# Kernel optimization log

Measured on AMD Instinct MI355X. Metric: run time of the kernel, lower is better.

## Reference

```python
import jax, jax.numpy as jnp
import numpy as np

B, T, D, A, H, NA = 32, 256, 1024, 64, 512, 20


def setup_inputs() -> dict:
    key = jax.random.key(0)
    ks = jax.random.split(key, 20)
    g = lambda i, sh: jax.random.normal(ks[i], sh, dtype=jnp.float32) * 0.05
    z = lambda sh: jnp.zeros(sh, jnp.float32)
    return dict(
        sentence=jax.random.normal(ks[0], (B, T, D), dtype=jnp.float32),
        actions=jax.random.randint(ks[1], (B, T), 0, NA),
        token_empty=g(2, (D,)),
        leaf_Wi=g(3, (D, D)), leaf_bi=z((D,)),
        leaf_Wo=g(4, (D, D)), leaf_bo=z((D,)),
        lstm_Wih=g(5, (4 * D, D)), lstm_Whh=g(6, (4 * D, D)),
        lstm_bih=z((4 * D,)), lstm_bhh=z((4 * D,)),
        stack_h0=g(7, (D,)), stack_c0=g(8, (D,)),
        act_emb=g(9, (NA, A)),
        act_Wih=g(10, (4 * D, A)), act_Whh=g(11, (4 * D, D)),
        act_bih=z((4 * D,)), act_bhh=z((4 * D,)),
        act_h0=g(12, (D,)), act_c0=g(13, (D,)),
        red_W=g(14, (4, D, 2 * D)), red_b=z((4, D)),
        h2f_W=g(15, (H, 8 * D)), h2f_b=z((H,)),
        f2a_W=g(16, (NA, H)), f2a_b=z((NA,)),
        att_W=g(17, (3, D, D)),
    )


def _lstm_cell(x, h, c, Wih, Whh, bih, bhh):
    # torch.nn.LSTMCell math
    gates = x @ Wih.T + bih + h @ Whh.T + bhh
    i, f, g, o = jnp.split(gates, 4, axis=-1)
    c2 = jax.nn.sigmoid(f) * c + jax.nn.sigmoid(i) * jnp.tanh(g)
    return jax.nn.sigmoid(o) * jnp.tanh(c2), c2


def _forward(sentence, token_empty, leaf_Wi, leaf_bi, leaf_Wo, leaf_bo,
             lstm_Wih, lstm_Whh, lstm_bih, lstm_bhh, stack_h0, stack_c0,
             act_emb, act_Wih, act_Whh, act_bih, act_bhh, act_h0, act_c0,
             red_W, red_b, h2f_W, h2f_b, f2a_W, f2a_b, att_W, actions):
    # _LeafModule on every token, vectorized: [B,T,D]
    cell = jnp.einsum('btd,ed->bte', sentence, leaf_Wi) + leaf_bi
    hid = jax.nn.sigmoid(jnp.einsum('btd,ed->bte', sentence, leaf_Wo) + leaf_bo) * jnp.tanh(cell)
    hid_t = jnp.swapaxes(hid, 0, 1)    # [T,B,D]
    cell_t = jnp.swapaxes(cell, 0, 1)

    # stack-LSTM: push every leaf hidden (SHIFT sequence)
    def stack_step(carry, x_t):
        h, c = carry
        h2, c2 = _lstm_cell(x_t, h, c, lstm_Wih, lstm_Whh, lstm_bih, lstm_bhh)
        return (h2, c2), h2
    init = (jnp.broadcast_to(stack_h0, (B, D)), jnp.broadcast_to(stack_c0, (B, D)))
    (hf, cf), stack_hs = jax.lax.scan(stack_step, init, hid_t)

    # _ReduceModule tree-LSTM, left-to-right binary reduce over all leaves
    def red_step(carry, rt):
        lh, lc = carry
        rh, rc = rt
        cat = jnp.concatenate([lh, rh], axis=-1)  # [B,2D]
        ig = jax.nn.sigmoid(cat @ red_W[0].T + red_b[0])
        lg = jax.nn.sigmoid(cat @ red_W[1].T + red_b[1])
        rg = jax.nn.sigmoid(cat @ red_W[2].T + red_b[2])
        cand = jnp.tanh(cat @ red_W[3].T + red_b[3])
        c2 = ig * cand + lg * lc + rg * rc
        return (jnp.tanh(c2), c2), None
    (red_h, _), _ = jax.lax.scan(red_step, (hid_t[0], cell_t[0]), (hid_t[1:], cell_t[1:]))

    # push the reduced node onto the stack-LSTM; top3 of the stack
    s1, _ = _lstm_cell(red_h, hf, cf, lstm_Wih, lstm_Whh, lstm_bih, lstm_bhh)
    s2, s3 = stack_hs[-1], stack_hs[-2]

    # action-LSTM over the action history
    a_in = jnp.swapaxes(act_emb[actions], 0, 1)  # [T,B,A]
    def act_step(carry, x_t):
        h, c = carry
        h2, c2 = _lstm_cell(x_t, h, c, act_Wih, act_Whh, act_bih, act_bhh)
        return (h2, c2), None
    ainit = (jnp.broadcast_to(act_h0, (B, D)), jnp.broadcast_to(act_c0, (B, D)))
    (a_top, _), _ = jax.lax.scan(act_step, ainit, a_in)

    # bilinear attention of each stack summary over the encoded sentence
    def bilin(s, W):
        w = jax.nn.softmax(jnp.einsum('bd,de,bte->bt', s, W, sentence), axis=-1)
        return jnp.einsum('bt,btd->bd', w, sentence)
    att1, att2, att3 = bilin(s1, att_W[0]), bilin(s2, att_W[1]), bilin(s3, att_W[2])

    buf_top = jnp.broadcast_to(token_empty, (B, D))  # buffer exhausted -> empty state
    feat = jnp.concatenate([s1, s2, s3, buf_top, a_top, att1, att2, att3], axis=-1)  # [B,8D]
    logits = jnp.tanh(feat @ h2f_W.T + h2f_b) @ f2a_W.T + f2a_b
    return jax.nn.log_softmax(logits, axis=-1)  # [B,NA]


def reference(sentence, actions, token_empty, leaf_Wi, leaf_bi, leaf_Wo, leaf_bo,
              lstm_Wih, lstm_Whh, lstm_bih, lstm_bhh, stack_h0, stack_c0,
              act_emb, act_Wih, act_Whh, act_bih, act_bhh, act_h0, act_c0,
              red_W, red_b, h2f_W, h2f_b, f2a_W, f2a_b, att_W):
    return _forward(sentence, token_empty, leaf_Wi, leaf_bi, leaf_Wo, leaf_bo,
                    lstm_Wih, lstm_Whh, lstm_bih, lstm_bhh, stack_h0, stack_c0,
                    act_emb, act_Wih, act_Whh, act_bih, act_bhh, act_h0, act_c0,
                    red_W, red_b, h2f_W, h2f_b, f2a_W, f2a_b, att_W, actions)
```

## Files before the change

### kernel.cpp

```cpp
#include <hip/hip_runtime.h>
#include <hip/hip_bf16.h>
#include <math.h>

#define DEV __device__ __forceinline__

typedef __bf16 bf16_t;
typedef bf16_t bf16x8 __attribute__((ext_vector_type(8)));
typedef float f32x4 __attribute__((ext_vector_type(4)));
typedef int i32x4 __attribute__((ext_vector_type(4)));

DEV void async16(const void* g, void* l) {
  __builtin_amdgcn_global_load_lds((const __attribute__((address_space(1))) void*)g,
                                   (__attribute__((address_space(3))) void*)l, 16, 0, 0);
}
DEV float sigmoidf_(float x) { return 1.f / (1.f + expf(-x)); }
DEV bf16x8 as_bf(i32x4 v) { union { i32x4 i; bf16x8 b; } u; u.i = v; return u.b; }

DEV unsigned flag_load(const unsigned* p) {
  unsigned v;
  asm volatile("global_load_dword %0, %1, off sc0 sc1\ns_waitcnt vmcnt(0)"
               : "=v"(v) : "v"(p) : "memory");
  return v;
}
DEV void flag_store(unsigned* p, unsigned v) {
  asm volatile("global_store_dword %0, %1, off sc0 sc1" :: "v"(p), "v"(v) : "memory");
}
DEV void store16_sys(void* p, i32x4 v) {
  asm volatile("global_store_dwordx4 %0, %1, off sc0 sc1" :: "v"(p), "v"(v) : "memory");
}

#define WAITV(N) do { asm volatile("s_waitcnt vmcnt(" #N ")" ::: "memory"); \
                      __builtin_amdgcn_sched_barrier(0); } while (0)

template<int KB>
DEV void loads8(i32x4* dst, const __hip_bfloat16* arow) {
#pragma unroll
  for (int i = 0; i < 8; ++i)
    asm volatile("global_load_dwordx4 %0, %1, off offset:%2"
                 : "=v"(dst[i]) : "v"(arow), "i"((KB + i) * 64));
}
DEV void loads8rt(i32x4* dst, const __hip_bfloat16* arow, int kbase) {
#pragma unroll
  for (int i = 0; i < 8; ++i)
    asm volatile("global_load_dwordx4 %0, %1, off"
                 : "=v"(dst[i]) : "v"(arow + (size_t)(kbase + i) * 32) : "memory");
}

template<int C>
DEV void ldsb8(bf16x8* b0, bf16x8* b1, const __hip_bfloat16* Wl,
               int sw, int kof, int r0, int r1) {
#pragma unroll
  for (int i = 0; i < 8; ++i) {
    const int kk = (C * 8 + i) * 32 + kof;
    b0[i] = *(const bf16x8*)&Wl[r0 * 1024 + (kk ^ sw)];
    b1[i] = *(const bf16x8*)&Wl[r1 * 1024 + (kk ^ sw)];
  }
}
DEV void mfma8x(const i32x4* a, const bf16x8* b0, const bf16x8* b1,
                f32x4& acc0, f32x4& acc1) {
#pragma unroll
  for (int i = 0; i < 8; ++i) {
    bf16x8 av = as_bf(a[i]);
    acc0 = __builtin_amdgcn_mfma_f32_16x16x32_bf16(av, b0[i], acc0, 0, 0, 0);
    acc1 = __builtin_amdgcn_mfma_f32_16x16x32_bf16(av, b1[i], acc1, 0, 0, 0);
  }
}

DEV void mfma_step(const __hip_bfloat16* Ap, const __hip_bfloat16* Wl,
                   int mh, int nh, int l, f32x4& acc0, f32x4& acc1) {
  const __hip_bfloat16* arow = Ap + (mh * 16 + (l & 15)) * 1024 + (l >> 4) * 8;
  const int sw = (l & 7) << 3, kof = (l >> 4) * 8;
  const int r0 = nh * 32 + (l & 15), r1 = r0 + 16;
  i32x4 A0[8], A1[8], A2[8], A3[8];
  bf16x8 Ba0[8], Ba1[8], Bb0[8], Bb1[8];
  loads8<0>(A0, arow);
  loads8<8>(A1, arow);
  loads8<16>(A2, arow);
  loads8<24>(A3, arow);
  ldsb8<0>(Ba0, Ba1, Wl, sw, kof, r0, r1);
  WAITV(24);
  mfma8x(A0, Ba0, Ba1, acc0, acc1);
  ldsb8<1>(Bb0, Bb1, Wl, sw, kof, r0, r1);
  WAITV(16);
  mfma8x(A1, Bb0, Bb1, acc0, acc1);
  ldsb8<2>(Ba0, Ba1, Wl, sw, kof, r0, r1);
  WAITV(8);
  mfma8x(A2, Ba0, Ba1, acc0, acc1);
  ldsb8<3>(Bb0, Bb1, Wl, sw, kof, r0, r1);
  WAITV(0);
  mfma8x(A3, Bb0, Bb1, acc0, acc1);
}

DEV void mfma_pass_glb(const __hip_bfloat16* Ap, const __hip_bfloat16* __restrict__ Wg,
                       int d0, int mh, int nh, int l, f32x4& acc0, f32x4& acc1) {
  const __hip_bfloat16* arow = Ap + (mh * 16 + (l & 15)) * 1024 + (l >> 4) * 8;
  const size_t g0 = ((size_t)(2 * nh) * 1024 + d0 + (l & 15)) * 1024;
  const size_t g1 = g0 + 1048576;
  const int kof = (l >> 4) * 8;
  i32x4 A[8];
  for (int c = 0; c < 4; ++c) {
    loads8rt(A, arow, c * 8);
    WAITV(0);
#pragma unroll
    for (int i = 0; i < 8; ++i) {
      const int kk = (c * 8 + i) * 32 + kof;
      bf16x8 b0 = *(const bf16x8*)&Wg[g0 + kk];
      bf16x8 b1 = *(const bf16x8*)&Wg[g1 + kk];
      bf16x8 av = as_bf(A[i]);
      acc0 = __builtin_amdgcn_mfma_f32_16x16x32_bf16(av, b0, acc0, 0, 0, 0);
      acc1 = __builtin_amdgcn_mfma_f32_16x16x32_bf16(av, b1, acc1, 0, 0, 0);
    }
  }
}

__global__ __launch_bounds__(256) void gemm_bt_kernel(
    const __hip_bfloat16* __restrict__ A, const __hip_bfloat16* __restrict__ Bw,
    float* __restrict__ outF, __hip_bfloat16* __restrict__ outBF,
    const float* __restrict__ bias, const float* __restrict__ aux,
    int M, int N, int K, int remap, int mode)
{
  __shared__ __hip_bfloat16 As[128 * 64];
  __shared__ __hip_bfloat16 Bs[128 * 64];
  __shared__ __hip_bfloat16 Cs[128 * 128];
  const int tid = threadIdx.x;
  const int w = tid >> 6, l = tid & 63;
  const int m0 = blockIdx.x * 128, n0 = blockIdx.y * 128;
  const int wm = (w >> 1) * 64, wn = (w & 1) * 64;
  const int row_s = tid >> 3, kc = tid & 7;
  f32x4 acc[4][4] = {};
  for (int k0 = 0; k0 < K; k0 += 64) {
    const __hip_bfloat16* ga = A + (size_t)(m0 + row_s) * K + k0 + kc * 8;
    const __hip_bfloat16* gb = Bw + (size_t)(n0 + row_s) * K + k0 + kc * 8;
    __hip_bfloat16* la = As + w * 512;
    __hip_bfloat16* lb = Bs + w * 512;
#pragma unroll
    for (int p = 0; p < 4; ++p) {
      async16(ga + (size_t)p * 32 * K, la + p * 2048);
      async16(gb + (size_t)p * 32 * K, lb + p * 2048);
    }
    __syncthreads();
#pragma unroll
    for (int kb = 0; kb < 2; ++kb) {
      bf16x8 af[4], bfr[4];
#pragma unroll
      for (int i = 0; i < 4; ++i)
        af[i] = *(const bf16x8*)&As[(wm + i * 16 + (l & 15)) * 64 + kb * 32 + (l >> 4) * 8];
#pragma unroll
      for (int j = 0; j < 4; ++j)
        bfr[j] = *(const bf16x8*)&Bs[(wn + j * 16 + (l & 15)) * 64 + kb * 32 + (l >> 4) * 8];
#pragma unroll
      for (int i = 0; i < 4; ++i)
#pragma unroll
        for (int j = 0; j < 4; ++j)
          acc[i][j] = __builtin_amdgcn_mfma_f32_16x16x32_bf16(af[i], bfr[j], acc[i][j], 0, 0, 0);
    }
    __syncthreads();
  }
  if (mode == 3) {
#pragma unroll
    for (int i = 0; i < 4; ++i)
#pragma unroll
      for (int j = 0; j < 4; ++j) {
        const int ncol = n0 + wn + j * 16 + (l & 15);
        const float bv = bias[ncol];
#pragma unroll
        for (int r = 0; r < 4; ++r) {
          const int lr = wm + i * 16 + (l >> 4) * 4 + r;
          Cs[lr * 128 + wn + j * 16 + (l & 15)] = __float2bfloat16(acc[i][j][r] + bv);
        }
      }
    __syncthreads();
    const int t0 = m0 >> 5, g = n0 >> 10, slot0 = (n0 & 1023) >> 4;
    const int grp = tid >> 6, li = tid & 63;
    const int b = li >> 1, half = li & 1;
#pragma unroll
    for (int sl = 0; sl < 8; ++sl) {
      bf16x8 vv = *(const bf16x8*)&Cs[(grp * 32 + b) * 128 + sl * 16 + half * 8];
      *(bf16x8*)&outBF[(((size_t)(slot0 + sl)) * 256 + t0 + grp) * 2048 +
                       g * 512 + b * 16 + half * 8] = vv;
    }
    return;
  }
#pragma unroll
  for (int i = 0; i < 4; ++i) {
#pragma unroll
    for (int j = 0; j < 4; ++j) {
      const int ncol = n0 + wn + j * 16 + (l & 15);
      const float bv = bias ? bias[ncol] : 0.f;
#pragma unroll
      for (int r = 0; r < 4; ++r) {
        int m = m0 + wm + i * 16 + (l >> 4) * 4 + r;
        int row = remap ? (((m & 255) << 5) | (m >> 8)) : m;
        float v = acc[i][j][r] + bv;
        if (mode == 0) {
          outF[(size_t)row * N + ncol] = v;
        } else if (mode == 1) {
          outBF[(size_t)row * N + ncol] = __float2bfloat16(v);
        } else {
          float cv = aux[(size_t)row * N + ncol];
          outBF[(size_t)row * N + ncol] = __float2bfloat16(sigmoidf_(v) * tanhf(cv));
        }
      }
    }
  }
}

__global__ __launch_bounds__(256) void cellblk_kernel(const float* __restrict__ cell,
                                                      __hip_bfloat16* __restrict__ blk)
{
  __shared__ __hip_bfloat16 ls[32 * 1024];
  const int t = blockIdx.x, tid = threadIdx.x;
  for (int i = tid; i < 32 * 1024; i += 256)
    ls[i] = __float2bfloat16(cell[(size_t)t * 32768 + i]);
  __syncthreads();
  const int e = tid * 2;
  const int b = e >> 4, dd = e & 15;
  for (int sl = 0; sl < 64; ++sl) {
    union { __hip_bfloat16 h[2]; unsigned u; } pk;
    pk.h[0] = ls[b * 1024 + sl * 16 + dd];
    pk.h[1] = ls[b * 1024 + sl * 16 + dd + 1];
    *(unsigned*)&blk[((size_t)sl * 256 + t) * 512 + e] = pk.u;
  }
}

struct PP {
  const __hip_bfloat16 *Whh_s, *Wih_s, *Whh_r, *Whh_a;
  const __hip_bfloat16 *xgs_blk, *xgr_blk;
  const __hip_bfloat16* cellblk;
  const float* table;
  const int* actions;
  const float *stack_c0, *act_c0, *sbias;
  __hip_bfloat16 *sh_hist, *rh_hist, *ah_hist;
  float *s1, *s2, *s3, *atop;
  unsigned int* flags;
};

__global__ __launch_bounds__(256, 1) void scan_persist(PP P)
{
  __shared__ __hip_bfloat16 Wl[64 * 1024];
  __shared__ float gsm[32][16][4];
  __shared__ __align__(16) __hip_bfloat16 hstage[32][16];
  const int bid = blockIdx.x;
  const int scan = bid >> 6;
  const int slot = bid & 63;
  const int d0 = slot * 16;
  const int tid = threadIdx.x;
  const int l = tid & 63, w = tid >> 6;
  const int mh = w >> 1, nh = w & 1;

  const __hip_bfloat16* Wg = (scan == 0) ? P.Whh_s : ((scan == 1) ? P.Whh_r : P.Whh_a);
  for (int idx = tid; idx < 64 * 128; idx += 256) {
    int r = idx >> 7, k = (idx & 127) * 8;
    int grow = ((r >> 4) << 10) + d0 + (r & 15);
    bf16x8 v = *(const bf16x8*)&Wg[(size_t)grow * 1024 + k];
    *(bf16x8*)&Wl[r * 1024 + (k ^ ((r & 7) << 3))] = v;
  }
  const int e0 = tid, e1 = tid + 256;
  const int b0_ = e0 >> 4, dd0 = e0 & 15, b1_ = e1 >> 4, dd1 = e1 & 15;
  float creg0, creg1;
  if (scan == 0)      { creg0 = P.stack_c0[d0 + dd0]; creg1 = P.stack_c0[d0 + dd1]; }
  else if (scan == 1) {
    creg0 = __bfloat162float(P.cellblk[(size_t)slot * 256 * 512 + b0_ * 16 + dd0]);
    creg1 = __bfloat162float(P.cellblk[(size_t)slot * 256 * 512 + b1_ * 16 + dd1]);
  }
  else                { creg0 = P.act_c0[d0 + dd0]; creg1 = P.act_c0[d0 + dd1]; }
  __syncthreads();

  __hip_bfloat16* hist = (scan == 0) ? P.sh_hist : ((scan == 1) ? P.rh_hist : P.ah_hist);
  unsigned int* Fb = P.flags + scan * 1024;
  const int Ns = (scan == 1) ? 255 : 256;
  const int mbase = mh * 16 + (l >> 4) * 4;

  for (int s = 0; s < Ns; ++s) {
    const __hip_bfloat16* Ap = hist + (size_t)s * 32768;
    __hip_bfloat16* Hout = hist + (size_t)(s + 1) * 32768;

    __hip_bfloat16 pg0, pg1, pg2, pg3, pg4, pg5, pg6, pg7;
    __hip_bfloat16 pcb0, pcb1;
    int pa0 = 0, pa1 = 0;
    pg0 = pg1 = pg2 = pg3 = pg4 = pg5 = pg6 = pg7 = __float2bfloat16(0.f);
    pcb0 = pcb1 = __float2bfloat16(0.f);
    if (scan == 0) {
      const __hip_bfloat16* x0 = P.xgs_blk + ((size_t)slot * 256 + s) * 2048 + b0_ * 16 + dd0;
      const __hip_bfloat16* x1 = P.xgs_blk + ((size_t)slot * 256 + s) * 2048 + b1_ * 16 + dd1;
      pg0 = x0[0]; pg1 = x0[512]; pg2 = x0[1024]; pg3 = x0[1536];
      pg4 = x1[0]; pg5 = x1[512]; pg6 = x1[1024]; pg7 = x1[1536];
    } else if (scan == 1) {
      const __hip_bfloat16* x0 = P.xgr_blk + ((size_t)slot * 256 + s + 1) * 2048 + b0_ * 16 + dd0;
      const __hip_bfloat16* x1 = P.xgr_blk + ((size_t)slot * 256 + s + 1) * 2048 + b1_ * 16 + dd1;
      pg0 = x0[0]; pg1 = x0[512]; pg2 = x0[1024]; pg3 = x0[1536];
      pg4 = x1[0]; pg5 = x1[512]; pg6 = x1[1024]; pg7 = x1[1536];
      pcb0 = P.cellblk[((size_t)slot * 256 + s + 1) * 512 + b0_ * 16 + dd0];
      pcb1 = P.cellblk[((size_t)slot * 256 + s + 1) * 512 + b1_ * 16 + dd1];
    } else {
      pa0 = P.actions[b0_ * 256 + s];
      pa1 = P.actions[b1_ * 256 + s];
    }
    __builtin_amdgcn_sched_barrier(0);

    f32x4 acc0 = {}, acc1 = {};
    mfma_step(Ap, Wl, mh, nh, l, acc0, acc1);
#pragma unroll
    for (int r = 0; r < 4; ++r) {
      gsm[mbase + r][l & 15][nh * 2 + 0] = acc0[r];
      gsm[mbase + r][l & 15][nh * 2 + 1] = acc1[r];
    }
    __syncthreads();
#pragma unroll
    for (int q = 0; q < 2; ++q) {
      const int b = q ? b1_ : b0_, dd = q ? dd1 : dd0;
      const int d = d0 + dd;
      float& creg = q ? creg1 : creg0;
      float g0 = gsm[b][dd][0], g1 = gsm[b][dd][1], g2 = gsm[b][dd][2], g3 = gsm[b][dd][3];
      if (scan == 1) {
        float ig = sigmoidf_(g0 + __bfloat162float(q ? pg4 : pg0));
        float lg = sigmoidf_(g1 + __bfloat162float(q ? pg5 : pg1));
        float rg = sigmoidf_(g2 + __bfloat162float(q ? pg6 : pg2));
        float cand = tanhf(g3 + __bfloat162float(q ? pg7 : pg3));
        float rcv = __bfloat162float(q ? pcb1 : pcb0);
        float c2 = ig * cand + lg * creg + rg * rcv;
        creg = c2;
        hstage[b][dd] = __float2bfloat16(tanhf(c2));
      } else {
        float bi0, bi1, bi2, bi3;
        if (scan == 0) {
          bi0 = __bfloat162float(q ? pg4 : pg0); bi1 = __bfloat162float(q ? pg5 : pg1);
          bi2 = __bfloat162float(q ? pg6 : pg2); bi3 = __bfloat162float(q ? pg7 : pg3);
        } else {
          int a = q ? pa1 : pa0;
          const float* tb = P.table + a * 4096;
          bi0 = tb[d]; bi1 = tb[1024 + d]; bi2 = tb[2048 + d]; bi3 = tb[3072 + d];
        }
        float c2 = sigmoidf_(g1 + bi1) * creg + sigmoidf_(g0 + bi0) * tanhf(g2 + bi2);
        float h2 = sigmoidf_(g3 + bi3) * tanhf(c2);
        creg = c2;
        hstage[b][dd] = __float2bfloat16(h2);
        if (scan == 0 && s == 254) P.s3[b * 1024 + d] = h2;
        if (scan == 0 && s == 255) P.s2[b * 1024 + d] = h2;
        if (scan == 2 && s == 255) P.atop[b * 1024 + d] = h2;
      }
    }
    __syncthreads();
    if (tid < 64) {
      const int bb = tid >> 1, hf = tid & 1;
      union { bf16x8 b8; i32x4 i4; } u;
      u.b8 = *(const bf16x8*)&hstage[bb][hf * 8];
      store16_sys(Hout + bb * 1024 + d0 + hf * 8, u.i4);
    }
    asm volatile("s_waitcnt vmcnt(0)" ::: "memory");
    __syncthreads();
    if (tid == 0) flag_store(Fb + slot * 16, (unsigned)(s + 1));
    if (tid < 64) {
      const unsigned tgt = (unsigned)(s + 1);
      if (flag_load(Fb + tid * 16) < tgt) {
        while (flag_load(Fb + tid * 16) < tgt) __builtin_amdgcn_s_sleep(1);
      }
    }
    __syncthreads();
  }

  if (scan == 0) {
    if (tid < 64) {
      while (flag_load(P.flags + 1024 + tid * 16) < 255u) __builtin_amdgcn_s_sleep(1);
    }
    __syncthreads();
    f32x4 acc0 = {}, acc1 = {};
    mfma_step(P.sh_hist + (size_t)256 * 32768, Wl, mh, nh, l, acc0, acc1);
    mfma_pass_glb(P.rh_hist + (size_t)255 * 32768, P.Wih_s, d0, mh, nh, l, acc0, acc1);
#pragma unroll
    for (int r = 0; r < 4; ++r) {
      gsm[mbase + r][l & 15][nh * 2 + 0] = acc0[r];
      gsm[mbase + r][l & 15][nh * 2 + 1] = acc1[r];
    }
    __syncthreads();
#pragma unroll
    for (int q = 0; q < 2; ++q) {
      const int b = q ? b1_ : b0_, dd = q ? dd1 : dd0;
      const int d = d0 + dd;
      float creg = q ? creg1 : creg0;
      float g0 = gsm[b][dd][0], g1 = gsm[b][dd][1], g2 = gsm[b][dd][2], g3 = gsm[b][dd][3];
      float bi0 = P.sbias[d], bi1 = P.sbias[1024 + d], bi2 = P.sbias[2048 + d], bi3 = P.sbias[3072 + d];
      float c2 = sigmoidf_(g1 + bi1) * creg + sigmoidf_(g0 + bi0) * tanhf(g2 + bi2);
      float h2 = sigmoidf_(g3 + bi3) * tanhf(c2);
      P.s1[b * 1024 + d] = h2;
    }
  }
}

__global__ void cast_kernel(__hip_bfloat16* dst, const float* src, int n) {
  int i = blockIdx.x * 256 + threadIdx.x;
  if (i < n) dst[i] = __float2bfloat16(src[i]);
}
__global__ void extract_half_kernel(__hip_bfloat16* dst, const float* src, int n,
                                    int src_stride, int src_off) {
  int i = blockIdx.x * 256 + threadIdx.x;
  if (i < n) {
    int r = i >> 10, k = i & 1023;
    dst[i] = __float2bfloat16(src[(size_t)r * src_stride + src_off + k]);
  }
}
__global__ void bias_kernel(float* dst, const float* a, const float* b, int n) {
  int i = blockIdx.x * 256 + threadIdx.x;
  if (i < n) dst[i] = a[i] + b[i];
}
__global__ void act_table_kernel(const float* emb, const float* Wih, const float* bih,
                                 const float* bhh, float* table) {
  int i = blockIdx.x * 256 + threadIdx.x;
  int a = i >> 12, n = i & 4095;
  float acc = bih[n] + bhh[n];
  const float* er = emb + a * 64;
  const float* wr = Wih + (size_t)n * 64;
  for (int k = 0; k < 64; ++k) acc += er[k] * wr[k];
  table[i] = acc;
}
__global__ void init_states_kernel(const float* stack_h0, const float* act_h0,
                                   const __hip_bfloat16* hid,
                                   __hip_bfloat16* sh0, __hip_bfloat16* ah0,
                                   __hip_bfloat16* rh0, unsigned int* flags)
{
  int i = blockIdx.x * 256 + threadIdx.x;
  int d = i & 1023;
  sh0[i] = __float2bfloat16(stack_h0[d]);
  ah0[i] = __float2bfloat16(act_h0[d]);
  rh0[i] = hid[i];
  if (i < 4096) flags[i] = 0u;
}

__global__ __launch_bounds__(256) void att_q_kernel(
    const float* s1, const float* s2, const float* s3, const float* attW, float* q)
{
  int eb = blockIdx.x, bg = blockIdx.y, j = blockIdx.z;
  const float* sj = (j == 0) ? s1 : ((j == 1) ? s2 : s3);
  __shared__ float ls[4][1024];
  int tid = threadIdx.x;
  for (int i = tid; i < 4096; i += 256)
    ls[i >> 10][i & 1023] = sj[(size_t)(bg * 4 + (i >> 10)) * 1024 + (i & 1023)];
  __syncthreads();
  int e = eb * 256 + tid;
  const float* Wj = attW + (size_t)j * 1024 * 1024;
  float a0 = 0, a1 = 0, a2 = 0, a3 = 0;
  for (int d = 0; d < 1024; ++d) {
    float wv = Wj[(size_t)d * 1024 + e];
    a0 += ls[0][d] * wv; a1 += ls[1][d] * wv; a2 += ls[2][d] * wv; a3 += ls[3][d] * wv;
  }
  q[((size_t)j * 32 + bg * 4 + 0) * 1024 + e] = a0;
  q[((size_t)j * 32 + bg * 4 + 1) * 1024 + e] = a1;
  q[((size_t)j * 32 + bg * 4 + 2) * 1024 + e] = a2;
  q[((size_t)j * 32 + bg * 4 + 3) * 1024 + e] = a3;
}

__global__ __launch_bounds__(256) void att_sc_kernel(const float* q, const float* sent, float* att)
{
  int b = blockIdx.x, j = blockIdx.y;
  __shared__ float qs[1024];
  __shared__ float wsm[256];
  __shared__ float red[8];
  int tid = threadIdx.x, w = tid >> 6, l = tid & 63;
  for (int i = tid; i < 1024; i += 256) qs[i] = q[((size_t)j * 32 + b) * 1024 + i];
  __syncthreads();
  const float* sp = sent + ((size_t)b * 256 + tid) * 1024;
  float dot = 0;
  for (int k = 0; k < 1024; ++k) dot += qs[k] * sp[k];
  float v = dot;
  for (int off = 32; off; off >>= 1) v = fmaxf(v, __shfl_xor(v, off));
  if (l == 0) red[w] = v;
  __syncthreads();
  float m = fmaxf(fmaxf(red[0], red[1]), fmaxf(red[2], red[3]));
  float ex = expf(dot - m);
  float sv = ex;
  for (int off = 32; off; off >>= 1) sv += __shfl_xor(sv, off);
  if (l == 0) red[4 + w] = sv;
  __syncthreads();
  float ssum = red[4] + red[5] + red[6] + red[7];
  wsm[tid] = ex / ssum;
  __syncthreads();
  for (int it = 0; it < 4; ++it) {
    int e = it * 256 + tid;
    float a = 0;
    for (int t2 = 0; t2 < 256; ++t2) a += wsm[t2] * sent[((size_t)b * 256 + t2) * 1024 + e];
    att[((size_t)j * 32 + b) * 1024 + e] = a;
  }
}

__global__ void feat_kernel(const float* s1, const float* s2, const float* s3,
                            const float* tok, const float* atop, const float* att, float* feat)
{
  int i = blockIdx.x * 256 + threadIdx.x;
  int b = i >> 13, jj = (i >> 10) & 7, d = i & 1023;
  int sidx = b * 1024 + d;
  float v;
  switch (jj) {
    case 0: v = s1[sidx]; break;
    case 1: v = s2[sidx]; break;
    case 2: v = s3[sidx]; break;
    case 3: v = tok[d]; break;
    case 4: v = atop[sidx]; break;
    default: v = att[((size_t)(jj - 5) * 32 + b) * 1024 + d];
  }
  feat[i] = v;
}
__global__ __launch_bounds__(256) void head_kernel(const float* feat, const float* W,
                                                   const float* bias, float* fbuf)
{
  int i = blockIdx.x * 256 + threadIdx.x;
  int b = i >> 9, h = i & 511;
  const float* fr = feat + (size_t)b * 8192;
  const float* wr = W + (size_t)h * 8192;
  float a = bias[h];
  for (int k = 0; k < 8192; ++k) a += fr[k] * wr[k];
  fbuf[i] = tanhf(a);
}
__global__ void logits_kernel(const float* fbuf, const float* W, const float* bias, float* out)
{
  int b = blockIdx.x, tid = threadIdx.x;
  __shared__ float lg[20];
  __shared__ float mred, lsred;
  if (tid < 20) {
    const float* fr = fbuf + b * 512;
    const float* wr = W + tid * 512;
    float a = bias[tid];
    for (int k = 0; k < 512; ++k) a += fr[k] * wr[k];
    lg[tid] = a;
  }
  __syncthreads();
  if (tid == 0) {
    float m = lg[0];
    for (int i = 1; i < 20; ++i) m = fmaxf(m, lg[i]);
    float ssum = 0;
    for (int i = 0; i < 20; ++i) ssum += expf(lg[i] - m);
    mred = m; lsred = logf(ssum);
  }
  __syncthreads();
  if (tid < 20) out[b * 20 + tid] = lg[tid] - mred - lsred;
}

extern "C" void kernel_launch(void* const* d_in, const int* in_sizes, int n_in,
                              void* d_out, int out_size, void* d_ws, size_t ws_size,
                              hipStream_t stream)
{
  const float* sentence = (const float*)d_in[0];
  const int* actions = (const int*)d_in[1];
  const float* token_empty = (const float*)d_in[2];
  const float* leaf_Wi = (const float*)d_in[3];
  const float* leaf_bi = (const float*)d_in[4];
  const float* leaf_Wo = (const float*)d_in[5];
  const float* leaf_bo = (const float*)d_in[6];
  const float* lstm_Wih = (const float*)d_in[7];
  const float* lstm_Whh = (const float*)d_in[8];
  const float* lstm_bih = (const float*)d_in[9];
  const float* lstm_bhh = (const float*)d_in[10];
  const float* stack_h0 = (const float*)d_in[11];
  const float* stack_c0 = (const float*)d_in[12];
  const float* act_emb = (const float*)d_in[13];
  const float* act_Wih = (const float*)d_in[14];
  const float* act_Whh = (const float*)d_in[15];
  const float* act_bih = (const float*)d_in[16];
  const float* act_bhh = (const float*)d_in[17];
  const float* act_h0 = (const float*)d_in[18];
  const float* act_c0 = (const float*)d_in[19];
  const float* red_W = (const float*)d_in[20];
  const float* red_b = (const float*)d_in[21];
  const float* h2f_W = (const float*)d_in[22];
  const float* h2f_b = (const float*)d_in[23];
  const float* f2a_W = (const float*)d_in[24];
  const float* f2a_b = (const float*)d_in[25];
  const float* att_W = (const float*)d_in[26];
  float* out = (float*)d_out;
  (void)in_sizes; (void)n_in; (void)out_size; (void)ws_size;

  char* ws = (char*)d_ws;
  size_t off = 0;
  auto alloc = [&](size_t bytes) -> void* {
    void* ptr = ws + off;
    off += (bytes + 255) & ~(size_t)255;
    return ptr;
  };
  char* arena = (char*)alloc(58720256);
  __hip_bfloat16* sent_bf = (__hip_bfloat16*)arena;
  float* cell_f32 = (float*)(arena + 16777216);
  __hip_bfloat16* Wx_r = (__hip_bfloat16*)(arena + 50331648);
  __hip_bfloat16* sh_hist = (__hip_bfloat16*)arena;
  __hip_bfloat16* rh_hist = (__hip_bfloat16*)(arena + 16843008);
  __hip_bfloat16* ah_hist = (__hip_bfloat16*)(arena + 33686016);

  __hip_bfloat16* hid_bf  = (__hip_bfloat16*)alloc(16777216);
  __hip_bfloat16* lWi_bf = (__hip_bfloat16*)alloc(2097152);
  __hip_bfloat16* lWo_bf = (__hip_bfloat16*)alloc(2097152);
  __hip_bfloat16* Whh_s = (__hip_bfloat16*)alloc(8388608);
  __hip_bfloat16* Wih_s = (__hip_bfloat16*)alloc(8388608);
  __hip_bfloat16* Whh_r = (__hip_bfloat16*)alloc(8388608);
  __hip_bfloat16* Whh_a = (__hip_bfloat16*)alloc(8388608);
  __hip_bfloat16* xgs_blk = (__hip_bfloat16*)alloc(67108864);
  __hip_bfloat16* xgr_blk = (__hip_bfloat16*)alloc(67108864);
  __hip_bfloat16* cellblk = (__hip_bfloat16*)alloc(16777216);
  float* table = (float*)alloc(327680);
  float* sbias = (float*)alloc(16384);
  float* s1 = (float*)alloc(131072);
  float* s2 = (float*)alloc(131072);
  float* s3 = (float*)alloc(131072);
  float* atop = (float*)alloc(131072);
  unsigned int* flags = (unsigned int*)alloc(16384);
  float* qbuf = (float*)alloc(393216);
  float* attbuf = (float*)alloc(393216);
  float* feat = (float*)alloc(1048576);
  float* fbuf = (float*)alloc(65536);

  cast_kernel<<<32768, 256, 0, stream>>>(sent_bf, sentence, 8388608);
  cast_kernel<<<4096, 256, 0, stream>>>(lWi_bf, leaf_Wi, 1048576);
  cast_kernel<<<4096, 256, 0, stream>>>(lWo_bf, leaf_Wo, 1048576);
  cast_kernel<<<16384, 256, 0, stream>>>(Whh_s, lstm_Whh, 4194304);
  cast_kernel<<<16384, 256, 0, stream>>>(Wih_s, lstm_Wih, 4194304);
  cast_kernel<<<16384, 256, 0, stream>>>(Whh_a, act_Whh, 4194304);
  extract_half_kernel<<<16384, 256, 0, stream>>>(Whh_r, red_W, 4194304, 2048, 0);
  extract_half_kernel<<<16384, 256, 0, stream>>>(Wx_r, red_W, 4194304, 2048, 1024);
  bias_kernel<<<16, 256, 0, stream>>>(sbias, lstm_bih, lstm_bhh, 4096);
  act_table_kernel<<<320, 256, 0, stream>>>(act_emb, act_Wih, act_bih, act_bhh, table);

  gemm_bt_kernel<<<dim3(64, 8), 256, 0, stream>>>(sent_bf, lWi_bf, cell_f32, nullptr,
                                                  leaf_bi, nullptr, 8192, 1024, 1024, 1, 0);
  gemm_bt_kernel<<<dim3(64, 8), 256, 0, stream>>>(sent_bf, lWo_bf, nullptr, hid_bf,
                                                  leaf_bo, cell_f32, 8192, 1024, 1024, 1, 2);
  cellblk_kernel<<<256, 256, 0, stream>>>(cell_f32, cellblk);

  gemm_bt_kernel<<<dim3(64, 32), 256, 0, stream>>>(hid_bf, Wih_s, nullptr, xgs_blk,
                                                   sbias, nullptr, 8192, 4096, 1024, 0, 3);
  gemm_bt_kernel<<<dim3(64, 32), 256, 0, stream>>>(hid_bf, Wx_r, nullptr, xgr_blk,
                                                   red_b, nullptr, 8192, 4096, 1024, 0, 3);

  init_states_kernel<<<128, 256, 0, stream>>>(stack_h0, act_h0, hid_bf,
                                              sh_hist, ah_hist, rh_hist, flags);

  PP P;
  P.Whh_s = Whh_s; P.Wih_s = Wih_s; P.Whh_r = Whh_r; P.Whh_a = Whh_a;
  P.xgs_blk = xgs_blk; P.xgr_blk = xgr_blk; P.cellblk = cellblk;
  P.table = table; P.actions = actions;
  P.stack_c0 = stack_c0; P.act_c0 = act_c0; P.sbias = sbias;
  P.sh_hist = sh_hist; P.rh_hist = rh_hist; P.ah_hist = ah_hist;
  P.s1 = s1; P.s2 = s2; P.s3 = s3; P.atop = atop;
  P.flags = flags;
  scan_persist<<<192, 256, 0, stream>>>(P);

  att_q_kernel<<<dim3(4, 8, 3), 256, 0, stream>>>(s1, s2, s3, att_W, qbuf);
  att_sc_kernel<<<dim3(32, 3), 256, 0, stream>>>(qbuf, sentence, attbuf);

  feat_kernel<<<1024, 256, 0, stream>>>(s1, s2, s3, token_empty, atop, attbuf, feat);
  head_kernel<<<64, 256, 0, stream>>>(feat, h2f_W, h2f_b, fbuf);
  logits_kernel<<<32, 64, 0, stream>>>(fbuf, f2a_W, f2a_b, out);
}
```

Baseline: 2.586 ms.

## Split flag wait by halves, prefetch A rows early, restructure gate LDS layout

Moves the per-step inter-block flag wait from the end of each step to the start of the next, and splits it into two halves. Loads of the first half of the A rows (batch-major hidden history) are issued as soon as the first 32 producer flags arrive, so global loads overlap with waiting for the remaining producers. The LDS-B fragment loads and MFMAs are software-pipelined by hand. The gate scratch array is transposed and padded to reduce bank conflicts. The head GEMV is vectorised with float4 loads and four independent accumulators. The synchronisation change relies on the mapping of rows to flags being correct. It adds a final wait on scan 0's own flags before the epilogue.

```diff
diff --git a/kernel.cpp b/kernel.cpp
--- a/kernel.cpp
+++ b/kernel.cpp
@@ -238,7 +238,7 @@
 __global__ __launch_bounds__(256, 1) void scan_persist(PP P)
 {
   __shared__ __hip_bfloat16 Wl[64 * 1024];
-  __shared__ float gsm[32][16][4];
+  __shared__ float gsm2[4][32][17];
   __shared__ __align__(16) __hip_bfloat16 hstage[32][16];
   const int bid = blockIdx.x;
   const int scan = bid >> 6;
@@ -270,6 +270,8 @@
   unsigned int* Fb = P.flags + scan * 1024;
   const int Ns = (scan == 1) ? 255 : 256;
   const int mbase = mh * 16 + (l >> 4) * 4;
+  const int sw = (l & 7) << 3, kof = (l >> 4) * 8;
+  const int r0 = nh * 32 + (l & 15), r1 = r0 + 16;
 
   for (int s = 0; s < Ns; ++s) {
     const __hip_bfloat16* Ap = hist + (size_t)s * 32768;
@@ -298,12 +300,45 @@
     }
     __builtin_amdgcn_sched_barrier(0);
 
+    if (s > 0 && tid < 32) {
+      const unsigned tgt = (unsigned)s;
+      if (flag_load(Fb + tid * 16) < tgt)
+        while (flag_load(Fb + tid * 16) < tgt) __builtin_amdgcn_s_sleep(1);
+    }
+    __syncthreads();
+
+    const __hip_bfloat16* arow = Ap + (mh * 16 + (l & 15)) * 1024 + kof;
+    i32x4 A0[8], A1[8], A2[8], A3[8];
+    loads8<0>(A0, arow);
+    loads8<8>(A1, arow);
+
+    if (s > 0 && tid < 32) {
+      const unsigned tgt = (unsigned)s;
+      if (flag_load(Fb + (32 + tid) * 16) < tgt)
+        while (flag_load(Fb + (32 + tid) * 16) < tgt) __builtin_amdgcn_s_sleep(1);
+    }
+    __syncthreads();
+    WAITV(0);
+    loads8<16>(A2, arow);
+    loads8<24>(A3, arow);
+
     f32x4 acc0 = {}, acc1 = {};
-    mfma_step(Ap, Wl, mh, nh, l, acc0, acc1);
+    bf16x8 Ba0[8], Ba1[8], Bb0[8], Bb1[8];
+    ldsb8<0>(Ba0, Ba1, Wl, sw, kof, r0, r1);
+    mfma8x(A0, Ba0, Ba1, acc0, acc1);
+    ldsb8<1>(Bb0, Bb1, Wl, sw, kof, r0, r1);
+    mfma8x(A1, Bb0, Bb1, acc0, acc1);
+    ldsb8<2>(Ba0, Ba1, Wl, sw, kof, r0, r1);
+    WAITV(8);
+    mfma8x(A2, Ba0, Ba1, acc0, acc1);
+    ldsb8<3>(Bb0, Bb1, Wl, sw, kof, r0, r1);
+    WAITV(0);
+    mfma8x(A3, Bb0, Bb1, acc0, acc1);
+
 #pragma unroll
     for (int r = 0; r < 4; ++r) {
-      gsm[mbase + r][l & 15][nh * 2 + 0] = acc0[r];
-      gsm[mbase + r][l & 15][nh * 2 + 1] = acc1[r];
+      gsm2[nh * 2 + 0][mbase + r][l & 15] = acc0[r];
+      gsm2[nh * 2 + 1][mbase + r][l & 15] = acc1[r];
     }
     __syncthreads();
 #pragma unroll
@@ -311,7 +346,7 @@
       const int b = q ? b1_ : b0_, dd = q ? dd1 : dd0;
       const int d = d0 + dd;
       float& creg = q ? creg1 : creg0;
-      float g0 = gsm[b][dd][0], g1 = gsm[b][dd][1], g2 = gsm[b][dd][2], g3 = gsm[b][dd][3];
+      float g0 = gsm2[0][b][dd], g1 = gsm2[1][b][dd], g2 = gsm2[2][b][dd], g3 = gsm2[3][b][dd];
       if (scan == 1) {
         float ig = sigmoidf_(g0 + __bfloat162float(q ? pg4 : pg0));
         float lg = sigmoidf_(g1 + __bfloat162float(q ? pg5 : pg1));
@@ -350,17 +385,11 @@
     asm volatile("s_waitcnt vmcnt(0)" ::: "memory");
     __syncthreads();
     if (tid == 0) flag_store(Fb + slot * 16, (unsigned)(s + 1));
-    if (tid < 64) {
-      const unsigned tgt = (unsigned)(s + 1);
-      if (flag_load(Fb + tid * 16) < tgt) {
-        while (flag_load(Fb + tid * 16) < tgt) __builtin_amdgcn_s_sleep(1);
-      }
-    }
-    __syncthreads();
   }
 
   if (scan == 0) {
     if (tid < 64) {
+      while (flag_load(P.flags + tid * 16) < 256u) __builtin_amdgcn_s_sleep(1);
       while (flag_load(P.flags + 1024 + tid * 16) < 255u) __builtin_amdgcn_s_sleep(1);
     }
     __syncthreads();
@@ -369,8 +398,8 @@
     mfma_pass_glb(P.rh_hist + (size_t)255 * 32768, P.Wih_s, d0, mh, nh, l, acc0, acc1);
 #pragma unroll
     for (int r = 0; r < 4; ++r) {
-      gsm[mbase + r][l & 15][nh * 2 + 0] = acc0[r];
-      gsm[mbase + r][l & 15][nh * 2 + 1] = acc1[r];
+      gsm2[nh * 2 + 0][mbase + r][l & 15] = acc0[r];
+      gsm2[nh * 2 + 1][mbase + r][l & 15] = acc1[r];
     }
     __syncthreads();
 #pragma unroll
@@ -378,7 +407,7 @@
       const int b = q ? b1_ : b0_, dd = q ? dd1 : dd0;
       const int d = d0 + dd;
       float creg = q ? creg1 : creg0;
-      float g0 = gsm[b][dd][0], g1 = gsm[b][dd][1], g2 = gsm[b][dd][2], g3 = gsm[b][dd][3];
+      float g0 = gsm2[0][b][dd], g1 = gsm2[1][b][dd], g2 = gsm2[2][b][dd], g3 = gsm2[3][b][dd];
       float bi0 = P.sbias[d], bi1 = P.sbias[1024 + d], bi2 = P.sbias[2048 + d], bi3 = P.sbias[3072 + d];
       float c2 = sigmoidf_(g1 + bi1) * creg + sigmoidf_(g0 + bi0) * tanhf(g2 + bi2);
       float h2 = sigmoidf_(g3 + bi3) * tanhf(c2);
@@ -504,11 +533,14 @@
 {
   int i = blockIdx.x * 256 + threadIdx.x;
   int b = i >> 9, h = i & 511;
-  const float* fr = feat + (size_t)b * 8192;
-  const float* wr = W + (size_t)h * 8192;
-  float a = bias[h];
-  for (int k = 0; k < 8192; ++k) a += fr[k] * wr[k];
-  fbuf[i] = tanhf(a);
+  const float4* fr = (const float4*)(feat + (size_t)b * 8192);
+  const float4* wr = (const float4*)(W + (size_t)h * 8192);
+  float a0 = 0, a1 = 0, a2 = 0, a3 = 0;
+  for (int k = 0; k < 2048; ++k) {
+    float4 f = fr[k], ww = wr[k];
+    a0 += f.x * ww.x; a1 += f.y * ww.y; a2 += f.z * ww.z; a3 += f.w * ww.w;
+  }
+  fbuf[i] = tanhf(bias[h] + ((a0 + a1) + (a2 + a3)));
 }
 __global__ void logits_kernel(const float* fbuf, const float* W, const float* bias, float* out)
 {
```

Result: no change. 2.553 ms (-1.3%).
